# Performance work log

Hardware: AMD Instinct MI355X
Metric: run time of the kernel (lower is better)

## Reference

```python
import jax, jax.numpy as jnp
import numpy as np

N, D = 32, 2                 # nodes, dof per node (dof_ndim)
BS = 4096
ZD = 2 * N * D               # state dim = 128
EDGE_I = np.arange(N - 1)    # chain edges (i, i+1)
EDGE_J = np.arange(1, N)
C = N                        # 1 tether + (N-1) distance constraints


def _minv(p, m_params):
    # point-mass (d2ids key 0) block mass-matrix inverse: diagonal per node
    inv_m = jnp.exp(-m_params[:, 0])            # (N,)
    return p * inv_m[:, None]


def _potential(r_flat, W0, b0, W1, b1, W2, b2, W3, b3):
    # V_net: mlp([N*D, h, h, h, 1], Softplus) followed by Reshape(-1)
    h = jax.nn.softplus(r_flat @ W0 + b0)
    h = jax.nn.softplus(h @ W1 + b1)
    h = jax.nn.softplus(h @ W2 + b2)
    return (h @ W3 + b3)[..., 0]                # (bs,)


def _hamiltonian(z, m_params, W0, b0, W1, b1, W2, b2, W3, b3):
    bs = z.shape[0]
    r = z[:, : ZD // 2].reshape(bs, N, D)
    p = z[:, ZD // 2 :].reshape(bs, N, D)
    T = 0.5 * jnp.sum(p * _minv(p, m_params), axis=(-1, -2))   # EuclideanT
    V = _potential(r.reshape(bs, -1), W0, b0, W1, b1, W2, b2, W3, b3)
    return T + V


def _rigid_dphi(r, v):
    # DPhi of shape (bs, 2, N, D, 2, C); axis1 = d/d(r,v), axis4 = (phi, phidot)
    # constraint 0: tether |r_0|^2 - l^2; constraints 1..N-1: |r_i - r_j|^2 - l^2
    bs = r.shape[0]
    dphi_dr = jnp.zeros((bs, N, D, C), r.dtype)
    dphidot_dr = jnp.zeros((bs, N, D, C), r.dtype)
    dphi_dr = dphi_dr.at[:, 0, :, 0].set(2.0 * r[:, 0])
    dphidot_dr = dphidot_dr.at[:, 0, :, 0].set(2.0 * v[:, 0])
    dr = 2.0 * (r[:, EDGE_I] - r[:, EDGE_J])    # (bs, N-1, D)
    dv = 2.0 * (v[:, EDGE_I] - v[:, EDGE_J])
    cidx = np.arange(1, N)
    dr_t = jnp.swapaxes(dr, 0, 1)               # (N-1, bs, D) for fancy-index scatter
    dv_t = jnp.swapaxes(dv, 0, 1)
    dphi_dr = dphi_dr.at[:, EDGE_I, :, cidx].add(dr_t)
    dphi_dr = dphi_dr.at[:, EDGE_J, :, cidx].add(-dr_t)
    dphidot_dr = dphidot_dr.at[:, EDGE_I, :, cidx].add(dv_t)
    dphidot_dr = dphidot_dr.at[:, EDGE_J, :, cidx].add(-dv_t)
    zeros = jnp.zeros_like(dphi_dr)
    d_r = jnp.stack([dphi_dr, dphidot_dr], axis=-2)   # (bs, N, D, 2, C)
    d_v = jnp.stack([zeros, dphi_dr], axis=-2)        # dphi/dv=0, dphidot/dv=dphi/dr
    return jnp.stack([d_r, d_v], axis=1)              # (bs, 2, N, D, 2, C)


def _chnn_dphi(z, m_params):
    bs = z.shape[0]
    zr = z.reshape(bs, 2, N, D)
    r, p = zr[:, 0], zr[:, 1]
    r_dot = _minv(p, m_params)
    DPhi = _rigid_dphi(r, r_dot)
    # convert velocity derivative to momentum derivative via Minv
    dv = _minv(DPhi[:, 1].reshape(bs, N, -1), m_params).reshape(DPhi[:, 1].shape)
    DPhi = jnp.stack([DPhi[:, 0], dv], axis=1)
    return DPhi.reshape(bs, 2 * N * D, -1)            # (bs, ZD, 2C)


def _J(M):
    # canonical symplectic map applied to column(s): J [a; b] = [b; -a]
    Dm = M.shape[-2]
    return jnp.concatenate([M[..., Dm // 2 :, :], -M[..., : Dm // 2, :]], axis=-2)


def setup_inputs() -> dict:
    key = jax.random.key(0)
    ks = jax.random.split(key, 8)
    return {
        "t": jnp.zeros((1,), jnp.float32),
        "z": jax.random.normal(ks[0], (BS, ZD), jnp.float32),
        "m_params": 0.1 * jax.random.normal(ks[1], (N, 1), jnp.float32),
        "W0": 0.1 * jax.random.normal(ks[2], (N * D, 256), jnp.float32),
        "b0": jnp.zeros((256,), jnp.float32),
        "W1": 0.1 * jax.random.normal(ks[3], (256, 256), jnp.float32),
        "b1": jnp.zeros((256,), jnp.float32),
        "W2": 0.1 * jax.random.normal(ks[4], (256, 256), jnp.float32),
        "b2": jnp.zeros((256,), jnp.float32),
        "W3": 0.1 * jax.random.normal(ks[5], (256, 1), jnp.float32),
        "b3": jnp.zeros((1,), jnp.float32),
    }


def reference(t, z, m_params, W0, b0, W1, b1, W2, b2, W3, b3):
    # constrained Hamiltonian vector field: P(J dH), P = I - J DPhi (DPhi^T J DPhi)^{-1} DPhi^T
    grad_H = jax.grad(
        lambda zz: _hamiltonian(zz, m_params, W0, b0, W1, b1, W2, b2, W3, b3).sum()
    )
    dH = grad_H(z)                          # (bs, ZD)
    DPhi = _chnn_dphi(z, m_params)          # (bs, ZD, 2C)
    JdH = _J(dH[..., None])                 # (bs, ZD, 1)
    DPhiT = jnp.swapaxes(DPhi, -1, -2)      # (bs, 2C, ZD)
    A = DPhiT @ _J(DPhi)                    # (bs, 2C, 2C)
    X = jnp.linalg.solve(A, DPhiT @ JdH)    # (bs, 2C, 1)
    return (JdH - _J(DPhi @ X))[..., 0]     # (bs, ZD)
```

## Files before the change

### kernel.cpp

```cpp
#include <hip/hip_runtime.h>

#define ZD   128
#define NP   32
#define SPB  16
#define NBLK (4096 / SPB)
#define NTH  512

typedef __attribute__((ext_vector_type(8))) short bf16x8;
typedef __attribute__((ext_vector_type(4))) float f32x4;

#define OFF_W0   0
#define OFF_W1   16384
#define OFF_W2   81920
#define OFF_W2T  147456
#define OFF_W1T  212992
#define OFF_W0T  278528
#define TOTE     294912

__device__ __forceinline__ float softplus_f(float x) {
    float e = __expf(-fabsf(x));
    return fmaxf(x, 0.0f) + __logf(1.0f + e);
}
__device__ __forceinline__ float sigmoid_f(float x) {
    return 1.0f / (1.0f + __expf(-x));
}
__device__ __forceinline__ unsigned short f2b(float f) {
    unsigned int u = __float_as_uint(f);
    unsigned int r = (u + 0x7FFFu + ((u >> 16) & 1u)) >> 16;
    return (unsigned short)r;
}
__device__ __forceinline__ float b2f(unsigned short h) {
    return __uint_as_float(((unsigned int)h) << 16);
}

__global__ void prep_pack(const float* __restrict__ W0,
                          const float* __restrict__ W1,
                          const float* __restrict__ W2,
                          short* __restrict__ P) {
    int T = blockIdx.x * 256 + threadIdx.x;
    if (T >= 36864) return;
    const float* src; int base, NT, trans, lu, t = T;
    if (t < 2048)               { src = W0; base = OFF_W0;  NT = 16; trans = 0; lu = t; }
    else if ((t -= 2048) < 8192){ src = W1; base = OFF_W1;  NT = 16; trans = 0; lu = t; }
    else if ((t -= 8192) < 8192){ src = W2; base = OFF_W2;  NT = 16; trans = 0; lu = t; }
    else if ((t -= 8192) < 8192){ src = W2; base = OFF_W2T; NT = 16; trans = 1; lu = t; }
    else if ((t -= 8192) < 8192){ src = W1; base = OFF_W1T; NT = 16; trans = 1; lu = t; }
    else              { t -= 8192; src = W0; base = OFF_W0T; NT = 4; trans = 1; lu = t; }
    int frag = lu >> 6, lane = lu & 63;
    int kb = frag / NT, nt = frag - kb * NT;
    int n  = nt * 16 + (lane & 15);
    int k0 = kb * 32 + ((lane >> 4) << 3);
    int N  = NT * 16;
    bf16x8 hv, lv;
    #pragma unroll
    for (int j = 0; j < 8; ++j) {
        int k = k0 + j;
        float w = trans ? src[n * 256 + k] : src[k * N + n];
        unsigned short h = f2b(w);
        unsigned short l = f2b(w - b2f(h));
        hv[j] = (short)h;
        lv[j] = (short)l;
    }
    ((bf16x8*)(P + base))[lu]        = hv;
    ((bf16x8*)(P + TOTE + base))[lu] = lv;
}

template<int KB, int NT, int TPW>
__device__ __forceinline__ void gemm_mf(const short* __restrict__ BH,
                                        const short* __restrict__ BL,
                                        const unsigned short (*aH)[264],
                                        const unsigned short (*aL)[264],
                                        int L, int quad, int wvx, f32x4* acc)
{
    #pragma unroll
    for (int kb = 0; kb < KB; ++kb) {
        bf16x8 ah = *(const bf16x8*)&aH[L & 15][kb * 32 + quad * 8];
        bf16x8 al = *(const bf16x8*)&aL[L & 15][kb * 32 + quad * 8];
        bf16x8 bh[TPW], bl[TPW];
        #pragma unroll
        for (int t = 0; t < TPW; ++t) {
            int frag = kb * NT + wvx * TPW + t;
            bh[t] = ((const bf16x8*)BH)[frag * 64 + L];
            bl[t] = ((const bf16x8*)BL)[frag * 64 + L];
        }
        #pragma unroll
        for (int t = 0; t < TPW; ++t) {
            acc[t] = __builtin_amdgcn_mfma_f32_16x16x32_bf16(ah, bh[t], acc[t], 0, 0, 0);
            acc[t] = __builtin_amdgcn_mfma_f32_16x16x32_bf16(ah, bl[t], acc[t], 0, 0, 0);
            acc[t] = __builtin_amdgcn_mfma_f32_16x16x32_bf16(al, bh[t], acc[t], 0, 0, 0);
        }
    }
}

__global__ __launch_bounds__(NTH, 2) void chnn_main(
    const float* __restrict__ z, const float* __restrict__ mp,
    const float* __restrict__ B0, const float* __restrict__ B1,
    const float* __restrict__ B2, const float* __restrict__ W3,
    const short* __restrict__ P,
    float* __restrict__ out)
{
    __shared__ __align__(16) unsigned short actH[2][16][264];
    __shared__ __align__(16) unsigned short actL[2][16][264];
    __shared__ __align__(16) float rsh[64][SPB];
    __shared__ __align__(16) float vsh[64][SPB];
    __shared__ __align__(16) float gsh[64][SPB];
    __shared__ float invm[NP];
    __shared__ double invmd[NP];
    __shared__ float ge[SPB][NP][2], gd[SPB][NP][2];
    __shared__ double Sdd[SPB][NP], Sed[SPB][NP], Ked[SPB][NP];
    __shared__ double b0d[SPB][NP], b1d[SPB][NP];
    __shared__ double wfac[SPB][NP], dinv[SPB][NP];

    const int tid  = threadIdx.x;
    const int L    = tid & 63;
    const int wv   = tid >> 6;
    const int quad = L >> 4;
    const long sbase = (long)blockIdx.x * SPB;

    const short* W0h  = P + OFF_W0;   const short* W0l  = P + TOTE + OFF_W0;
    const short* W1h  = P + OFF_W1;   const short* W1l  = P + TOTE + OFF_W1;
    const short* W2h  = P + OFF_W2;   const short* W2l  = P + TOTE + OFF_W2;
    const short* W2Th = P + OFF_W2T;  const short* W2Tl = P + TOTE + OFF_W2T;
    const short* W1Th = P + OFF_W1T;  const short* W1Tl = P + TOTE + OFF_W1T;
    const short* W0Th = P + OFF_W0T;  const short* W0Tl = P + TOTE + OFF_W0T;

    if (tid < NP) {
        double e = exp(-(double)mp[tid]);
        invmd[tid] = e;
        invm[tid] = (float)e;
    }

    const float* zb = z + sbase * ZD;
    #pragma unroll
    for (int k = 0; k < 4; ++k) {
        int e = k * NTH + tid;
        int s = e >> 7, idx = e & 127;
        float val = zb[e];
        if (idx < 64) {
            rsh[idx][s] = val;
            unsigned short h = f2b(val);
            actH[0][s][idx] = h;
            actL[0][s][idx] = f2b(val - b2f(h));
        } else {
            vsh[idx - 64][s] = val;
        }
    }
    __syncthreads();
    {
        float* pv = &vsh[0][0];
        #pragma unroll
        for (int k = 0; k < 2; ++k) {
            int e = k * NTH + tid;
            pv[e] *= invm[e >> 5];
        }
    }
    __syncthreads();

    f32x4 acc[2];
    float p0s[2][4], p1s[2][4];
    const int nbase = wv * 32 + (L & 15);

    #pragma unroll
    for (int t = 0; t < 2; ++t) {
        float bb = B0[nbase + t * 16];
        acc[t] = (f32x4){bb, bb, bb, bb};
    }
    gemm_mf<2, 16, 2>(W0h, W0l, actH[0], actL[0], L, quad, wv, acc);
    #pragma unroll
    for (int t = 0; t < 2; ++t) {
        int n = nbase + t * 16;
        #pragma unroll
        for (int r = 0; r < 4; ++r) {
            p0s[t][r] = acc[t][r];
            int m = quad * 4 + r;
            float h = softplus_f(acc[t][r]);
            unsigned short hh = f2b(h);
            actH[1][m][n] = hh;
            actL[1][m][n] = f2b(h - b2f(hh));
        }
    }
    __syncthreads();

    #pragma unroll
    for (int t = 0; t < 2; ++t) {
        float bb = B1[nbase + t * 16];
        acc[t] = (f32x4){bb, bb, bb, bb};
    }
    gemm_mf<8, 16, 2>(W1h, W1l, actH[1], actL[1], L, quad, wv, acc);
    #pragma unroll
    for (int t = 0; t < 2; ++t) {
        int n = nbase + t * 16;
        #pragma unroll
        for (int r = 0; r < 4; ++r) {
            p1s[t][r] = acc[t][r];
            int m = quad * 4 + r;
            float h = softplus_f(acc[t][r]);
            unsigned short hh = f2b(h);
            actH[0][m][n] = hh;
            actL[0][m][n] = f2b(h - b2f(hh));
        }
    }
    __syncthreads();

    #pragma unroll
    for (int t = 0; t < 2; ++t) {
        float bb = B2[nbase + t * 16];
        acc[t] = (f32x4){bb, bb, bb, bb};
    }
    gemm_mf<8, 16, 2>(W2h, W2l, actH[0], actL[0], L, quad, wv, acc);
    #pragma unroll
    for (int t = 0; t < 2; ++t) {
        int n = nbase + t * 16;
        float w3 = W3[n];
        #pragma unroll
        for (int r = 0; r < 4; ++r) {
            int m = quad * 4 + r;
            float h = w3 * sigmoid_f(acc[t][r]);
            unsigned short hh = f2b(h);
            actH[1][m][n] = hh;
            actL[1][m][n] = f2b(h - b2f(hh));
        }
    }
    __syncthreads();

    #pragma unroll
    for (int t = 0; t < 2; ++t) acc[t] = (f32x4){0.f, 0.f, 0.f, 0.f};
    gemm_mf<8, 16, 2>(W2Th, W2Tl, actH[1], actL[1], L, quad, wv, acc);
    #pragma unroll
    for (int t = 0; t < 2; ++t) {
        int n = nbase + t * 16;
        #pragma unroll
        for (int r = 0; r < 4; ++r) {
            int m = quad * 4 + r;
            float h = acc[t][r] * sigmoid_f(p1s[t][r]);
            unsigned short hh = f2b(h);
            actH[0][m][n] = hh;
            actL[0][m][n] = f2b(h - b2f(hh));
        }
    }
    __syncthreads();

    #pragma unroll
    for (int t = 0; t < 2; ++t) acc[t] = (f32x4){0.f, 0.f, 0.f, 0.f};
    gemm_mf<8, 16, 2>(W1Th, W1Tl, actH[0], actL[0], L, quad, wv, acc);
    #pragma unroll
    for (int t = 0; t < 2; ++t) {
        int n = nbase + t * 16;
        #pragma unroll
        for (int r = 0; r < 4; ++r) {
            int m = quad * 4 + r;
            float h = acc[t][r] * sigmoid_f(p0s[t][r]);
            unsigned short hh = f2b(h);
            actH[1][m][n] = hh;
            actL[1][m][n] = f2b(h - b2f(hh));
        }
    }
    __syncthreads();

    if (wv < 4) {
        acc[0] = (f32x4){0.f, 0.f, 0.f, 0.f};
        gemm_mf<8, 4, 1>(W0Th, W0Tl, actH[1], actL[1], L, quad, wv, acc);
        int i = wv * 16 + (L & 15);
        #pragma unroll
        for (int r = 0; r < 4; ++r) {
            int m = quad * 4 + r;
            gsh[i][m] = acc[0][r];
        }
    }
    __syncthreads();

    {
        const int c = tid & 31;
        const int s = tid >> 5;
        double gx, gy, gdx, gdy;
        if (c == 0) {
            double r0x = rsh[0][s], r0y = rsh[1][s];
            double v0x = vsh[0][s], v0y = vsh[1][s];
            gx = 2.0 * r0x; gy = 2.0 * r0y; gdx = 2.0 * v0x; gdy = 2.0 * v0y;
            Sdd[s][0] = invmd[0] * (gx * gx + gy * gy);
            b0d[s][0] = gx * v0x + gy * v0y;
            b1d[s][0] = gdx * v0x + gdy * v0y
                      - invmd[0] * (gx * (double)gsh[0][s] + gy * (double)gsh[1][s]);
        } else {
            int aa = 2 * (c - 1), b = 2 * c;
            double dvx = (double)vsh[aa][s] - (double)vsh[b][s];
            double dvy = (double)vsh[aa + 1][s] - (double)vsh[b + 1][s];
            gx = 2.0 * ((double)rsh[aa][s] - (double)rsh[b][s]);
            gy = 2.0 * ((double)rsh[aa + 1][s] - (double)rsh[b + 1][s]);
            gdx = 2.0 * dvx; gdy = 2.0 * dvy;
            Sdd[s][c] = (invmd[c - 1] + invmd[c]) * (gx * gx + gy * gy);
            b0d[s][c] = gx * dvx + gy * dvy;
            double mgx = invmd[c - 1] * (double)gsh[aa][s]     - invmd[c] * (double)gsh[b][s];
            double mgy = invmd[c - 1] * (double)gsh[aa + 1][s] - invmd[c] * (double)gsh[b + 1][s];
            b1d[s][c] = gdx * dvx + gdy * dvy - (gx * mgx + gy * mgy);
        }
        ge[s][c][0] = (float)gx;  ge[s][c][1] = (float)gy;
        gd[s][c][0] = (float)gdx; gd[s][c][1] = (float)gdy;
        __syncthreads();
        if (c < 31) {
            double g1x = ge[s][c + 1][0], g1y = ge[s][c + 1][1];
            double q1x = gd[s][c + 1][0], q1y = gd[s][c + 1][1];
            if (c == 0) {
                Sed[s][0] = invmd[0] * (gx * g1x + gy * g1y);
                Ked[s][0] = invmd[0] * ((gdx * g1x + gdy * g1y) - (gx * q1x + gy * q1y));
            } else {
                Sed[s][c] = -invmd[c] * (gx * g1x + gy * g1y);
                Ked[s][c] =  invmd[c] * ((gx * q1x + gy * q1y) - (gdx * g1x + gdy * g1y));
            }
        }
    }
    __syncthreads();

    if (tid < SPB) {
        int s = tid;
        double d = Sdd[s][0];
        if (d == 0.0) d = 1e-300;
        dinv[s][0] = 1.0 / d;
        double y = b0d[s][0];
        for (int c = 1; c < NP; ++c) {
            double e = Sed[s][c - 1];
            double w = e * dinv[s][c - 1];
            wfac[s][c - 1] = w;
            d = Sdd[s][c] - w * e;
            if (d == 0.0) d = 1e-300;
            dinv[s][c] = 1.0 / d;
            y = b0d[s][c] - w * y;
            b0d[s][c] = y;
        }
        double x = b0d[s][31] * dinv[s][31];
        b0d[s][31] = x;
        for (int c = 30; c >= 0; --c) {
            x = (b0d[s][c] - Sed[s][c] * x) * dinv[s][c];
            b0d[s][c] = x;
        }
    }
    __syncthreads();

    {
        int c = tid & 31, s = tid >> 5;
        double kx = 0.0;
        if (c < 31) kx += Ked[s][c] * b0d[s][c + 1];
        if (c > 0)  kx -= Ked[s][c - 1] * b0d[s][c - 1];
        b1d[s][c] = kx - b1d[s][c];
    }
    __syncthreads();

    if (tid < SPB) {
        int s = tid;
        double y = b1d[s][0];
        for (int c = 1; c < NP; ++c) {
            y = b1d[s][c] - wfac[s][c - 1] * y;
            b1d[s][c] = y;
        }
        double x = b1d[s][31] * dinv[s][31];
        b1d[s][31] = x;
        for (int c = 30; c >= 0; --c) {
            x = (b1d[s][c] - Sed[s][c] * x) * dinv[s][c];
            b1d[s][c] = x;
        }
    }
    __syncthreads();

    float* ob = out + sbase * ZD;
    #pragma unroll
    for (int k = 0; k < 4; ++k) {
        int e = k * NTH + tid;
        int s = e >> 7, idx = e & 127;
        int j = idx & 63;
        int n = j >> 1, d = j & 1;
        float res;
        if (idx < 64) {
            double Gx1 = (n == 0) ? (double)ge[s][0][d] * b0d[s][0]
                                  : -(double)ge[s][n][d] * b0d[s][n];
            if (n < 31) Gx1 += (double)ge[s][n + 1][d] * b0d[s][n + 1];
            res = (float)((double)vsh[j][s] - invmd[n] * Gx1);
        } else {
            double Gx0 = (n == 0) ? (double)ge[s][0][d] * b1d[s][0]
                                  : -(double)ge[s][n][d] * b1d[s][n];
            if (n < 31) Gx0 += (double)ge[s][n + 1][d] * b1d[s][n + 1];
            double Gd1 = (n == 0) ? (double)gd[s][0][d] * b0d[s][0]
                                  : -(double)gd[s][n][d] * b0d[s][n];
            if (n < 31) Gd1 += (double)gd[s][n + 1][d] * b0d[s][n + 1];
            res = (float)(-(double)gsh[j][s] + Gx0 + Gd1);
        }
        ob[e] = res;
    }
}

extern "C" void kernel_launch(void* const* d_in, const int* in_sizes, int n_in,
                              void* d_out, int out_size, void* d_ws, size_t ws_size,
                              hipStream_t stream) {
    const float* z  = (const float*)d_in[1];
    const float* mp = (const float*)d_in[2];
    const float* W0 = (const float*)d_in[3];
    const float* B0 = (const float*)d_in[4];
    const float* W1 = (const float*)d_in[5];
    const float* B1 = (const float*)d_in[6];
    const float* W2 = (const float*)d_in[7];
    const float* B2 = (const float*)d_in[8];
    const float* W3 = (const float*)d_in[9];

    short* P = (short*)d_ws;

    prep_pack<<<144, 256, 0, stream>>>(W0, W1, W2, P);
    chnn_main<<<NBLK, NTH, 0, stream>>>(z, mp, B0, B1, B2, W3, P, (float*)d_out);
}
```

Before: 114.9 us.

## Drop split-bf16 emulation and prefetch next-layer weight fragments into registers

Replaces the three-MFMA hi/lo bf16 split (an emulation of fp32 accuracy) with a single plain bf16 MFMA per tile. This removes the low-part weight and activation buffers along with their conversions. It also double-buffers weight fragments in registers so the next layer's B operands load from global memory while the current layer computes. The cost is lower precision in the MLP gradient, which feeds the constraint projection and may exceed the tolerance, and higher register pressure from 32 fragment registers.

```diff
diff --git a/kernel.cpp b/kernel.cpp
--- a/kernel.cpp
+++ b/kernel.cpp
@@ -15,7 +15,6 @@
 #define OFF_W2T  147456
 #define OFF_W1T  212992
 #define OFF_W0T  278528
-#define TOTE     294912
 
 __device__ __forceinline__ float softplus_f(float x) {
     float e = __expf(-fabsf(x));
@@ -28,9 +27,6 @@
     unsigned int u = __float_as_uint(f);
     unsigned int r = (u + 0x7FFFu + ((u >> 16) & 1u)) >> 16;
     return (unsigned short)r;
-}
-__device__ __forceinline__ float b2f(unsigned short h) {
-    return __uint_as_float(((unsigned int)h) << 16);
 }
 
 __global__ void prep_pack(const float* __restrict__ W0,
@@ -51,44 +47,37 @@
     int n  = nt * 16 + (lane & 15);
     int k0 = kb * 32 + ((lane >> 4) << 3);
     int N  = NT * 16;
-    bf16x8 hv, lv;
+    bf16x8 hv;
     #pragma unroll
     for (int j = 0; j < 8; ++j) {
         int k = k0 + j;
         float w = trans ? src[n * 256 + k] : src[k * N + n];
-        unsigned short h = f2b(w);
-        unsigned short l = f2b(w - b2f(h));
-        hv[j] = (short)h;
-        lv[j] = (short)l;
-    }
-    ((bf16x8*)(P + base))[lu]        = hv;
-    ((bf16x8*)(P + TOTE + base))[lu] = lv;
+        hv[j] = (short)f2b(w);
+    }
+    ((bf16x8*)(P + base))[lu] = hv;
 }
 
 template<int KB, int NT, int TPW>
-__device__ __forceinline__ void gemm_mf(const short* __restrict__ BH,
-                                        const short* __restrict__ BL,
-                                        const unsigned short (*aH)[264],
-                                        const unsigned short (*aL)[264],
-                                        int L, int quad, int wvx, f32x4* acc)
-{
+__device__ __forceinline__ void load_B(const short* __restrict__ BH,
+                                       int L, int wvx, bf16x8* dst) {
+    #pragma unroll
+    for (int kb = 0; kb < KB; ++kb)
+        #pragma unroll
+        for (int t = 0; t < TPW; ++t)
+            dst[kb * TPW + t] = ((const bf16x8*)BH)[(kb * NT + wvx * TPW + t) * 64 + L];
+}
+
+template<int KB, int TPW>
+__device__ __forceinline__ void mfma_B(const unsigned short (*aH)[264],
+                                       int L, int quad,
+                                       const bf16x8* fr, f32x4* acc) {
     #pragma unroll
     for (int kb = 0; kb < KB; ++kb) {
         bf16x8 ah = *(const bf16x8*)&aH[L & 15][kb * 32 + quad * 8];
-        bf16x8 al = *(const bf16x8*)&aL[L & 15][kb * 32 + quad * 8];
-        bf16x8 bh[TPW], bl[TPW];
-        #pragma unroll
-        for (int t = 0; t < TPW; ++t) {
-            int frag = kb * NT + wvx * TPW + t;
-            bh[t] = ((const bf16x8*)BH)[frag * 64 + L];
-            bl[t] = ((const bf16x8*)BL)[frag * 64 + L];
-        }
-        #pragma unroll
-        for (int t = 0; t < TPW; ++t) {
-            acc[t] = __builtin_amdgcn_mfma_f32_16x16x32_bf16(ah, bh[t], acc[t], 0, 0, 0);
-            acc[t] = __builtin_amdgcn_mfma_f32_16x16x32_bf16(ah, bl[t], acc[t], 0, 0, 0);
-            acc[t] = __builtin_amdgcn_mfma_f32_16x16x32_bf16(al, bh[t], acc[t], 0, 0, 0);
-        }
+        #pragma unroll
+        for (int t = 0; t < TPW; ++t)
+            acc[t] = __builtin_amdgcn_mfma_f32_16x16x32_bf16(ah, fr[kb * TPW + t],
+                                                             acc[t], 0, 0, 0);
     }
 }
 
@@ -100,7 +89,6 @@
     float* __restrict__ out)
 {
     __shared__ __align__(16) unsigned short actH[2][16][264];
-    __shared__ __align__(16) unsigned short actL[2][16][264];
     __shared__ __align__(16) float rsh[64][SPB];
     __shared__ __align__(16) float vsh[64][SPB];
     __shared__ __align__(16) float gsh[64][SPB];
@@ -117,18 +105,14 @@
     const int quad = L >> 4;
     const long sbase = (long)blockIdx.x * SPB;
 
-    const short* W0h  = P + OFF_W0;   const short* W0l  = P + TOTE + OFF_W0;
-    const short* W1h  = P + OFF_W1;   const short* W1l  = P + TOTE + OFF_W1;
-    const short* W2h  = P + OFF_W2;   const short* W2l  = P + TOTE + OFF_W2;
-    const short* W2Th = P + OFF_W2T;  const short* W2Tl = P + TOTE + OFF_W2T;
-    const short* W1Th = P + OFF_W1T;  const short* W1Tl = P + TOTE + OFF_W1T;
-    const short* W0Th = P + OFF_W0T;  const short* W0Tl = P + TOTE + OFF_W0T;
-
     if (tid < NP) {
         double e = exp(-(double)mp[tid]);
         invmd[tid] = e;
         invm[tid] = (float)e;
     }
+
+    bf16x8 frA[16], frB[16];
+    load_B<2, 16, 2>(P + OFF_W0, L, wv, frA);
 
     const float* zb = z + sbase * ZD;
     #pragma unroll
@@ -138,9 +122,7 @@
         float val = zb[e];
         if (idx < 64) {
             rsh[idx][s] = val;
-            unsigned short h = f2b(val);
-            actH[0][s][idx] = h;
-            actL[0][s][idx] = f2b(val - b2f(h));
+            actH[0][s][idx] = f2b(val);
         } else {
             vsh[idx - 64][s] = val;
         }
@@ -160,112 +142,92 @@
     float p0s[2][4], p1s[2][4];
     const int nbase = wv * 32 + (L & 15);
 
+    load_B<8, 16, 2>(P + OFF_W1, L, wv, frB);
     #pragma unroll
     for (int t = 0; t < 2; ++t) {
         float bb = B0[nbase + t * 16];
         acc[t] = (f32x4){bb, bb, bb, bb};
     }
-    gemm_mf<2, 16, 2>(W0h, W0l, actH[0], actL[0], L, quad, wv, acc);
+    mfma_B<2, 2>(actH[0], L, quad, frA, acc);
     #pragma unroll
     for (int t = 0; t < 2; ++t) {
         int n = nbase + t * 16;
         #pragma unroll
         for (int r = 0; r < 4; ++r) {
             p0s[t][r] = acc[t][r];
-            int m = quad * 4 + r;
-            float h = softplus_f(acc[t][r]);
-            unsigned short hh = f2b(h);
-            actH[1][m][n] = hh;
-            actL[1][m][n] = f2b(h - b2f(hh));
-        }
-    }
-    __syncthreads();
-
+            actH[1][quad * 4 + r][n] = f2b(softplus_f(acc[t][r]));
+        }
+    }
+    __syncthreads();
+
+    load_B<8, 16, 2>(P + OFF_W2, L, wv, frA);
     #pragma unroll
     for (int t = 0; t < 2; ++t) {
         float bb = B1[nbase + t * 16];
         acc[t] = (f32x4){bb, bb, bb, bb};
     }
-    gemm_mf<8, 16, 2>(W1h, W1l, actH[1], actL[1], L, quad, wv, acc);
+    mfma_B<8, 2>(actH[1], L, quad, frB, acc);
     #pragma unroll
     for (int t = 0; t < 2; ++t) {
         int n = nbase + t * 16;
         #pragma unroll
         for (int r = 0; r < 4; ++r) {
             p1s[t][r] = acc[t][r];
-            int m = quad * 4 + r;
-            float h = softplus_f(acc[t][r]);
-            unsigned short hh = f2b(h);
-            actH[0][m][n] = hh;
-            actL[0][m][n] = f2b(h - b2f(hh));
-        }
-    }
-    __syncthreads();
-
+            actH[0][quad * 4 + r][n] = f2b(softplus_f(acc[t][r]));
+        }
+    }
+    __syncthreads();
+
+    load_B<8, 16, 2>(P + OFF_W2T, L, wv, frB);
     #pragma unroll
     for (int t = 0; t < 2; ++t) {
         float bb = B2[nbase + t * 16];
         acc[t] = (f32x4){bb, bb, bb, bb};
     }
-    gemm_mf<8, 16, 2>(W2h, W2l, actH[0], actL[0], L, quad, wv, acc);
+    mfma_B<8, 2>(actH[0], L, quad, frA, acc);
     #pragma unroll
     for (int t = 0; t < 2; ++t) {
         int n = nbase + t * 16;
         float w3 = W3[n];
         #pragma unroll
-        for (int r = 0; r < 4; ++r) {
-            int m = quad * 4 + r;
-            float h = w3 * sigmoid_f(acc[t][r]);
-            unsigned short hh = f2b(h);
-            actH[1][m][n] = hh;
-            actL[1][m][n] = f2b(h - b2f(hh));
-        }
-    }
-    __syncthreads();
-
+        for (int r = 0; r < 4; ++r)
+            actH[1][quad * 4 + r][n] = f2b(w3 * sigmoid_f(acc[t][r]));
+    }
+    __syncthreads();
+
+    load_B<8, 16, 2>(P + OFF_W1T, L, wv, frA);
     #pragma unroll
     for (int t = 0; t < 2; ++t) acc[t] = (f32x4){0.f, 0.f, 0.f, 0.f};
-    gemm_mf<8, 16, 2>(W2Th, W2Tl, actH[1], actL[1], L, quad, wv, acc);
-    #pragma unroll
-    for (int t = 0; t < 2; ++t) {
-        int n = nbase + t * 16;
-        #pragma unroll
-        for (int r = 0; r < 4; ++r) {
-            int m = quad * 4 + r;
-            float h = acc[t][r] * sigmoid_f(p1s[t][r]);
-            unsigned short hh = f2b(h);
-            actH[0][m][n] = hh;
-            actL[0][m][n] = f2b(h - b2f(hh));
-        }
-    }
-    __syncthreads();
-
+    mfma_B<8, 2>(actH[1], L, quad, frB, acc);
+    #pragma unroll
+    for (int t = 0; t < 2; ++t) {
+        int n = nbase + t * 16;
+        #pragma unroll
+        for (int r = 0; r < 4; ++r)
+            actH[0][quad * 4 + r][n] = f2b(acc[t][r] * sigmoid_f(p1s[t][r]));
+    }
+    __syncthreads();
+
+    if (wv < 4) load_B<8, 4, 1>(P + OFF_W0T, L, wv, frB);
     #pragma unroll
     for (int t = 0; t < 2; ++t) acc[t] = (f32x4){0.f, 0.f, 0.f, 0.f};
-    gemm_mf<8, 16, 2>(W1Th, W1Tl, actH[0], actL[0], L, quad, wv, acc);
-    #pragma unroll
-    for (int t = 0; t < 2; ++t) {
-        int n = nbase + t * 16;
-        #pragma unroll
-        for (int r = 0; r < 4; ++r) {
-            int m = quad * 4 + r;
-            float h = acc[t][r] * sigmoid_f(p0s[t][r]);
-            unsigned short hh = f2b(h);
-            actH[1][m][n] = hh;
-            actL[1][m][n] = f2b(h - b2f(hh));
-        }
+    mfma_B<8, 2>(actH[0], L, quad, frA, acc);
+    #pragma unroll
+    for (int t = 0; t < 2; ++t) {
+        int n = nbase + t * 16;
+        #pragma unroll
+        for (int r = 0; r < 4; ++r)
+            actH[1][quad * 4 + r][n] = f2b(acc[t][r] * sigmoid_f(p0s[t][r]));
     }
     __syncthreads();
 
     if (wv < 4) {
         acc[0] = (f32x4){0.f, 0.f, 0.f, 0.f};
-        gemm_mf<8, 4, 1>(W0Th, W0Tl, actH[1], actL[1], L, quad, wv, acc);
+        mfma_B<8, 1>(actH[1], L, quad, frB, acc);
         int i = wv * 16 + (L & 15);
         #pragma unroll
-        for (int r = 0; r < 4; ++r) {
-            int m = quad * 4 + r;
-            gsh[i][m] = acc[0][r];
-        }
+        for (int r = 0; r < 4; ++r)
+            gsh[i][quad * 4 + r] = acc[0][r];
     }
     __syncthreads();
 
```

Result: faster. 94.52 us (median of 2 runs) (-17.8%).
